# Performance work log

Hardware: AMD Instinct MI355X
Metric: run time of the kernel (lower is better)

The kernel has to match this reference:

```python
import jax, jax.numpy as jnp
import numpy as np

N_NODES = 100000
NEG_SLOPE = 0.01  # F.leaky_relu default


def _hetero_graphconv(x, src, dst, W, b, n_nodes):
    """HeteroGraphConv(aggregate='sum') of DGL GraphConv(norm='both') per edge type.

    x: [N, d_in]; src/dst: [R, E] int; W: [R, d_in, d_out]; b: [R, d_out].
    """
    n_rel = W.shape[0]
    ones = None
    out = jnp.zeros((n_nodes, W.shape[2]), dtype=x.dtype)
    for r in range(n_rel):  # small fixed number of relations
        s, d = src[r], dst[r]
        e_ones = jnp.ones(s.shape, dtype=x.dtype)
        deg_out = jnp.clip(jax.ops.segment_sum(e_ones, s, num_segments=n_nodes), 1.0)
        deg_in = jnp.clip(jax.ops.segment_sum(e_ones, d, num_segments=n_nodes), 1.0)
        # norm='both': scale src by out_deg^-1/2, aggregate, scale dst by in_deg^-1/2.
        # Apply weight before gather (aggregation is linear) to shrink edge traffic.
        h = (x * (deg_out ** -0.5)[:, None]) @ W[r]          # [N, d_out]
        agg = jax.ops.segment_sum(h[s], d, num_segments=n_nodes)  # gather-scatter over edges
        out = out + agg * (deg_in ** -0.5)[:, None] + b[r]
    return out


def setup_inputs() -> dict:
    key = jax.random.key(0)
    ks = jax.random.split(key, 8)
    d_in, d_h, d_out, n_cls, n_rel, n_edges = 256, 128, 128, 16, 3, 600000
    x = jax.random.normal(ks[0], (N_NODES, d_in), dtype=jnp.float32)
    src = jax.random.randint(ks[1], (n_rel, n_edges), 0, N_NODES, dtype=jnp.int32)
    dst = jax.random.randint(ks[2], (n_rel, n_edges), 0, N_NODES, dtype=jnp.int32)
    W0 = jax.random.normal(ks[3], (n_rel, d_in, d_h), dtype=jnp.float32) * (d_in ** -0.5)
    b0 = jnp.zeros((n_rel, d_h), dtype=jnp.float32)
    W1 = jax.random.normal(ks[4], (n_rel, d_h, d_out), dtype=jnp.float32) * (d_h ** -0.5)
    b1 = jnp.zeros((n_rel, d_out), dtype=jnp.float32)
    fc_W = jax.random.normal(ks[5], (d_out, n_cls), dtype=jnp.float32) * (d_out ** -0.5)
    fc_b = jnp.zeros((n_cls,), dtype=jnp.float32)
    return {"x": x, "src": src, "dst": dst, "W0": W0, "b0": b0,
            "W1": W1, "b1": b1, "fc_W": fc_W, "fc_b": fc_b}


def reference(x, src, dst, W0, b0, W1, b1, fc_W, fc_b):
    n = x.shape[0]
    h = _hetero_graphconv(x, src, dst, W0, b0, n)
    h = jax.nn.leaky_relu(h, negative_slope=NEG_SLOPE)  # dropout rate 0 (eval)
    h = _hetero_graphconv(h, src, dst, W1, b1, n)       # last layer: no activation
    logits = h @ fc_W + fc_b
    return (h, logits)
```

## Files before the change

### kernel.cpp

```cpp
#include <hip/hip_runtime.h>
#include <hip/hip_bf16.h>
#include <stdint.h>


typedef __attribute__((ext_vector_type(8))) short bf16x8;
typedef __attribute__((ext_vector_type(4))) float f32x4;
typedef unsigned short u16;

#define SCAN_T 256
#define SCAN_E 8
#define SCAN_BLK (SCAN_T * SCAN_E)

__global__ __launch_bounds__(256)
void hist_kernel(const int* __restrict__ src, const int* __restrict__ dst,
                 int* __restrict__ cnt_out8, int* __restrict__ cnt_in8,
                 int E, int N) {
    int e = blockIdx.x * blockDim.x + threadIdx.x;
    int r = blockIdx.y;
    if (e >= E) return;
    int copy = blockIdx.x & 7;
    size_t base = ((size_t)copy * 3 + r) * N;
    atomicAdd(cnt_out8 + base + src[(size_t)r * E + e], 1);
    atomicAdd(cnt_in8  + base + dst[(size_t)r * E + e], 1);
}

__global__ __launch_bounds__(256)
void reduce_scales_kernel(const int* __restrict__ cnt_out8, const int* __restrict__ cnt_in8,
                          float* __restrict__ s_out, float* __restrict__ s_in,
                          int* __restrict__ cnt_in, int total ) {
    int i = blockIdx.x * blockDim.x + threadIdx.x;
    if (i >= total) return;
    int co = 0, ci = 0;
#pragma unroll
    for (int c = 0; c < 8; c++) {
        co += cnt_out8[(size_t)c * total + i];
        ci += cnt_in8[(size_t)c * total + i];
    }
    s_out[i] = rsqrtf(fmaxf((float)co, 1.0f));
    s_in[i]  = rsqrtf(fmaxf((float)ci, 1.0f));
    cnt_in[i] = ci;
}

__global__ __launch_bounds__(SCAN_T)
void scan1_kernel(const int* __restrict__ cnt, int* __restrict__ pre,
                  int* __restrict__ bsums, int N) {
    int r = blockIdx.y, b = blockIdx.x, t = threadIdx.x;
    int base = b * SCAN_BLK + t * SCAN_E;
    int v[SCAN_E], s = 0;
#pragma unroll
    for (int j = 0; j < SCAN_E; j++) {
        int idx = base + j;
        v[j] = (idx < N) ? cnt[(size_t)r * N + idx] : 0;
        s += v[j];
    }
    __shared__ int sd[SCAN_T];
    sd[t] = s;
    __syncthreads();
    for (int off = 1; off < SCAN_T; off <<= 1) {
        int x = (t >= off) ? sd[t - off] : 0;
        __syncthreads();
        sd[t] += x;
        __syncthreads();
    }
    if (t == SCAN_T - 1) bsums[r * gridDim.x + b] = sd[t];
    int run = sd[t] - s;
#pragma unroll
    for (int j = 0; j < SCAN_E; j++) {
        int idx = base + j;
        if (idx < N) pre[(size_t)r * (N + 1) + idx] = run;
        run += v[j];
    }
}

__global__ void scan2_kernel(int* __restrict__ bsums, int* __restrict__ row_start,
                             int nb, int N) {
    for (int r = 0; r < 3; r++) {
        int run = 0;
        for (int b = 0; b < nb; b++) {
            int t = bsums[r * nb + b];
            bsums[r * nb + b] = run;
            run += t;
        }
        row_start[(size_t)r * (N + 1) + N] = run;
    }
}

__global__ __launch_bounds__(SCAN_T)
void scan3_kernel(int* __restrict__ pre, const int* __restrict__ bsums,
                  int* __restrict__ cursor, int nb, int N) {
    int r = blockIdx.y, b = blockIdx.x, t = threadIdx.x;
    int add = bsums[r * nb + b];
    int base = b * SCAN_BLK + t * SCAN_E;
#pragma unroll
    for (int j = 0; j < SCAN_E; j++) {
        int idx = base + j;
        if (idx < N) {
            int val = pre[(size_t)r * (N + 1) + idx] + add;
            pre[(size_t)r * (N + 1) + idx] = val;
            cursor[(size_t)r * N + idx] = val;
        }
    }
}

__global__ __launch_bounds__(256)
void bucket_fill_kernel(const int* __restrict__ src, const int* __restrict__ dst,
                        int* __restrict__ cursor, int* __restrict__ esrc,
                        int E, int N) {
    int e = blockIdx.x * blockDim.x + threadIdx.x;
    int r = blockIdx.y;
    if (e >= E) return;
    int d = dst[(size_t)r * E + e];
    int pos = atomicAdd(cursor + (size_t)r * N + d, 1);
    esrc[(size_t)r * E + pos] = src[(size_t)r * E + e];
}

__global__ __launch_bounds__(256)
void prep_w_kernel(const float* __restrict__ W0, const float* __restrict__ W1,
                   u16* __restrict__ w0hi, u16* __restrict__ w0lo,
                   u16* __restrict__ w1hi, u16* __restrict__ w1lo) {
    int idx = blockIdx.x * blockDim.x + threadIdx.x;
    const int n0 = 3 * 256 * 128;
    const int n1 = 3 * 128 * 128;
    if (idx >= n0 + n1) return;
    float f;
    u16 *phi, *plo;
    int oidx;
    if (idx < n0) {
        int r = idx / 32768, rem = idx % 32768;
        int n = rem / 256, k = rem % 256;
        f = W0[(size_t)r * 32768 + (size_t)k * 128 + n];
        phi = w0hi; plo = w0lo; oidx = idx;
    } else {
        int i2 = idx - n0;
        int r = i2 / 16384, rem = i2 % 16384;
        int n = rem / 128, k = rem % 128;
        f = W1[(size_t)r * 16384 + (size_t)k * 128 + n];
        phi = w1hi; plo = w1lo; oidx = i2;
    }
    uint32_t u = __float_as_uint(f);
    phi[oidx] = (u16)(u >> 16);
    float lo = f - __uint_as_float(u & 0xFFFF0000u);
    uint32_t ul = __float_as_uint(lo);
    plo[oidx] = (u16)((ul + 0x7FFFu + ((ul >> 16) & 1u)) >> 16);
}

__global__ __launch_bounds__(256)
void gemm_split_bf16(const float* __restrict__ A, const float* __restrict__ s_out,
                     const u16* __restrict__ Whi_all, const u16* __restrict__ Wlo_all,
                     u16* __restrict__ Cout_all, int M, int K, int Nn) {
    const int r = blockIdx.y;
    const float* scale = s_out + (size_t)r * Nn;
    const u16* Whi = Whi_all + (size_t)r * K * 128;
    const u16* Wlo = Wlo_all + (size_t)r * K * 128;
    u16* Cout = Cout_all + (size_t)r * Nn * 128;

    __shared__ u16 As_hi[128][40];
    __shared__ u16 As_lo[128][40];
    __shared__ u16 Bs_hi[128][40];
    __shared__ u16 Bs_lo[128][40];

    const int tid  = threadIdx.x;
    const int m0   = blockIdx.x * 128;
    const int lane = tid & 63;
    const int wave = tid >> 6;
    const int wm   = (wave & 1) * 64;
    const int wn   = (wave >> 1) * 64;
    const int lm   = lane & 15;
    const int kq   = (lane >> 4) * 8;

    f32x4 acc[4][4];
#pragma unroll
    for (int i = 0; i < 4; i++)
#pragma unroll
        for (int j = 0; j < 4; j++) acc[i][j] = (f32x4){0.f, 0.f, 0.f, 0.f};

    const int srow = tid >> 1;
    const int skb  = (tid & 1) * 16;

    const bool valid = (m0 + srow) < M;
    const float sval = valid ? scale[m0 + srow] : 0.f;
    const float* arow = A + (size_t)(m0 + srow) * K;
    const u16* whrow = Whi + (size_t)srow * K;
    const u16* wlrow = Wlo + (size_t)srow * K;

    for (int k0 = 0; k0 < K; k0 += 32) {
        float fa[16];
        if (valid) {
            *(float4*)&fa[0]  = *(const float4*)(arow + k0 + skb);
            *(float4*)&fa[4]  = *(const float4*)(arow + k0 + skb + 4);
            *(float4*)&fa[8]  = *(const float4*)(arow + k0 + skb + 8);
            *(float4*)&fa[12] = *(const float4*)(arow + k0 + skb + 12);
        } else {
#pragma unroll
            for (int i = 0; i < 16; i++) fa[i] = 0.f;
        }
        uint32_t ah[8], al[8];
#pragma unroll
        for (int p = 0; p < 8; p++) {
            float f0 = fa[2 * p] * sval, f1 = fa[2 * p + 1] * sval;
            uint32_t u0 = __float_as_uint(f0), u1 = __float_as_uint(f1);
            ah[p] = (u0 >> 16) | (u1 & 0xFFFF0000u);
            float l0 = f0 - __uint_as_float(u0 & 0xFFFF0000u);
            float l1 = f1 - __uint_as_float(u1 & 0xFFFF0000u);
            al[p] = (__float_as_uint(l0) >> 16) | (__float_as_uint(l1) & 0xFFFF0000u);
        }
        *(uint4*)&As_hi[srow][skb]     = *(uint4*)&ah[0];
        *(uint4*)&As_hi[srow][skb + 8] = *(uint4*)&ah[4];
        *(uint4*)&As_lo[srow][skb]     = *(uint4*)&al[0];
        *(uint4*)&As_lo[srow][skb + 8] = *(uint4*)&al[4];

        *(uint4*)&Bs_hi[srow][skb]     = *(const uint4*)(whrow + k0 + skb);
        *(uint4*)&Bs_hi[srow][skb + 8] = *(const uint4*)(whrow + k0 + skb + 8);
        *(uint4*)&Bs_lo[srow][skb]     = *(const uint4*)(wlrow + k0 + skb);
        *(uint4*)&Bs_lo[srow][skb + 8] = *(const uint4*)(wlrow + k0 + skb + 8);

        __syncthreads();

        bf16x8 a_hi[4], a_lo[4], b_hi[4], b_lo[4];
#pragma unroll
        for (int i = 0; i < 4; i++) {
            a_hi[i] = *(const bf16x8*)&As_hi[wm + i * 16 + lm][kq];
            a_lo[i] = *(const bf16x8*)&As_lo[wm + i * 16 + lm][kq];
            b_hi[i] = *(const bf16x8*)&Bs_hi[wn + i * 16 + lm][kq];
            b_lo[i] = *(const bf16x8*)&Bs_lo[wn + i * 16 + lm][kq];
        }
#pragma unroll
        for (int i = 0; i < 4; i++)
#pragma unroll
            for (int j = 0; j < 4; j++) {
                acc[i][j] = __builtin_amdgcn_mfma_f32_16x16x32_bf16(a_hi[i], b_hi[j], acc[i][j], 0, 0, 0);
                acc[i][j] = __builtin_amdgcn_mfma_f32_16x16x32_bf16(a_lo[i], b_hi[j], acc[i][j], 0, 0, 0);
                acc[i][j] = __builtin_amdgcn_mfma_f32_16x16x32_bf16(a_hi[i], b_lo[j], acc[i][j], 0, 0, 0);
            }
        __syncthreads();
    }

    const int rq = (lane >> 4) * 4;
#pragma unroll
    for (int i = 0; i < 4; i++) {
        int mbase = m0 + wm + i * 16 + rq;
#pragma unroll
        for (int j = 0; j < 4; j++) {
            int col = wn + j * 16 + lm;
#pragma unroll
            for (int rg = 0; rg < 4; rg++) {
                int m = mbase + rg;
                if (m < M) {
                    uint32_t u = __float_as_uint(acc[i][j][rg]);
                    Cout[(size_t)m * 128 + col] =
                        (u16)((u + 0x7FFFu + ((u >> 16) & 1u)) >> 16);
                }
            }
        }
    }
}

#define BF16_LO(u) __uint_as_float((u) << 16)
#define BF16_HI(u) __uint_as_float((u) & 0xFFFF0000u)

__device__ __forceinline__ void gather_rel(const uint32_t* __restrict__ h,
                                           const int* __restrict__ es,
                                           int beg, int end,
                                           float& ox, float& oy, float w) {
    float ax = 0.f, ay = 0.f, cx = 0.f, cy = 0.f;
    int e = beg;
    for (; e + 4 <= end; e += 4) {
        int s0 = es[e], s1 = es[e + 1], s2 = es[e + 2], s3 = es[e + 3];
        uint32_t u0 = h[(size_t)s0 * 64];
        uint32_t u1 = h[(size_t)s1 * 64];
        uint32_t u2 = h[(size_t)s2 * 64];
        uint32_t u3 = h[(size_t)s3 * 64];
        ax += BF16_LO(u0); ay += BF16_HI(u0);
        cx += BF16_LO(u1); cy += BF16_HI(u1);
        ax += BF16_LO(u2); ay += BF16_HI(u2);
        cx += BF16_LO(u3); cy += BF16_HI(u3);
    }
    if (e + 2 <= end) {
        int s0 = es[e], s1 = es[e + 1];
        uint32_t u0 = h[(size_t)s0 * 64];
        uint32_t u1 = h[(size_t)s1 * 64];
        ax += BF16_LO(u0); ay += BF16_HI(u0);
        cx += BF16_LO(u1); cy += BF16_HI(u1);
        e += 2;
    }
    if (e < end) {
        uint32_t u0 = h[(size_t)es[e] * 64];
        ax += BF16_LO(u0); ay += BF16_HI(u0);
    }
    ox += (ax + cx) * w;
    oy += (ay + cy) * w;
}

__global__ __launch_bounds__(256)
void gather_l0(const u16* __restrict__ hb, const int* __restrict__ row_start,
               const int* __restrict__ esrc, const float* __restrict__ s_in,
               const float* __restrict__ b, float* __restrict__ out, int N, int E) {
    int node = blockIdx.x * 4 + (threadIdx.x >> 6);
    if (node >= N) return;
    int lane = threadIdx.x & 63;
    float tx = 0.f, ty = 0.f;
#pragma unroll
    for (int r = 0; r < 3; r++) {
        const int* rs = row_start + (size_t)r * (N + 1);
        gather_rel((const uint32_t*)hb + (size_t)r * N * 64 + lane,
                   esrc + (size_t)r * E, rs[node], rs[node + 1],
                   tx, ty, s_in[(size_t)r * N + node]);
    }
    int c0 = lane * 2;
    tx += b[c0] + b[128 + c0] + b[256 + c0];
    ty += b[c0 + 1] + b[128 + c0 + 1] + b[256 + c0 + 1];
    tx = fmaxf(tx, 0.f) + 0.01f * fminf(tx, 0.f);
    ty = fmaxf(ty, 0.f) + 0.01f * fminf(ty, 0.f);
    *(float2*)(out + (size_t)node * 128 + c0) = make_float2(tx, ty);
}

__global__ __launch_bounds__(256)
void gather_l1(const u16* __restrict__ hb, const int* __restrict__ row_start,
               const int* __restrict__ esrc, const float* __restrict__ s_in,
               const float* __restrict__ b, const float* __restrict__ fcW,
               const float* __restrict__ fcb, float* __restrict__ out_h,
               float* __restrict__ out_logits, int N, int E) {
    int node = blockIdx.x * 4 + (threadIdx.x >> 6);
    if (node >= N) return;
    int lane = threadIdx.x & 63;
    float tx = 0.f, ty = 0.f;
#pragma unroll
    for (int r = 0; r < 3; r++) {
        const int* rs = row_start + (size_t)r * (N + 1);
        gather_rel((const uint32_t*)hb + (size_t)r * N * 64 + lane,
                   esrc + (size_t)r * E, rs[node], rs[node + 1],
                   tx, ty, s_in[(size_t)r * N + node]);
    }
    int c0 = lane * 2;
    tx += b[c0] + b[128 + c0] + b[256 + c0];
    ty += b[c0 + 1] + b[128 + c0 + 1] + b[256 + c0 + 1];
    *(float2*)(out_h + (size_t)node * 128 + c0) = make_float2(tx, ty);

    const float* fc0 = fcW + (size_t)c0 * 16;
    float p[16];
#pragma unroll
    for (int j = 0; j < 16; j++) p[j] = tx * fc0[j] + ty * fc0[16 + j];
#pragma unroll
    for (int off = 1; off < 64; off <<= 1) {
#pragma unroll
        for (int j = 0; j < 16; j++) p[j] += __shfl_xor(p[j], off);
    }
    if (lane == 0) {
        float* lp = out_logits + (size_t)node * 16;
        *(float4*)(lp + 0)  = make_float4(p[0] + fcb[0],  p[1] + fcb[1],  p[2] + fcb[2],  p[3] + fcb[3]);
        *(float4*)(lp + 4)  = make_float4(p[4] + fcb[4],  p[5] + fcb[5],  p[6] + fcb[6],  p[7] + fcb[7]);
        *(float4*)(lp + 8)  = make_float4(p[8] + fcb[8],  p[9] + fcb[9],  p[10] + fcb[10], p[11] + fcb[11]);
        *(float4*)(lp + 12) = make_float4(p[12] + fcb[12], p[13] + fcb[13], p[14] + fcb[14], p[15] + fcb[15]);
    }
}

extern "C" void kernel_launch(void* const* d_in, const int* in_sizes, int n_in,
                              void* d_out, int out_size, void* d_ws, size_t ws_size,
                              hipStream_t stream) {
    const float* x   = (const float*)d_in[0];
    const int*   src = (const int*)d_in[1];
    const int*   dst = (const int*)d_in[2];
    const float* W0  = (const float*)d_in[3];
    const float* b0  = (const float*)d_in[4];
    const float* W1  = (const float*)d_in[5];
    const float* b1  = (const float*)d_in[6];
    const float* fcW = (const float*)d_in[7];
    const float* fcb = (const float*)d_in[8];

    const int N = in_sizes[0] / 256;
    const int E = in_sizes[1] / 3;
    const int nb = (N + SCAN_BLK - 1) / SCAN_BLK;

    float* out_h      = (float*)d_out;
    float* out_logits = out_h + (size_t)N * 128;

    char* p = (char*)d_ws;
    auto alloc = [&](size_t bytes) -> char* {
        char* q = p;
        p += (bytes + 255) & ~(size_t)255;
        return q;
    };
    float* s_out     = (float*)alloc(3 * (size_t)N * 4);
    float* s_in      = (float*)alloc(3 * (size_t)N * 4);
    int*   cnt8      = (int*)alloc(2 * 8 * 3 * (size_t)N * 4);
    int*   cnt_out8  = cnt8;
    int*   cnt_in8   = cnt8 + 8 * 3 * (size_t)N;
    int*   cnt_in    = (int*)alloc(3 * (size_t)N * 4);
    int*   row_start = (int*)alloc(3 * (size_t)(N + 1) * 4);
    int*   cursor    = (int*)alloc(3 * (size_t)N * 4);
    int*   bsums     = (int*)alloc(1024 * 4);
    int*   esrc      = (int*)alloc(3 * (size_t)E * 4);
    u16*   w0hi      = (u16*)alloc(3 * 256 * 128 * 2);
    u16*   w0lo      = (u16*)alloc(3 * 256 * 128 * 2);
    u16*   w1hi      = (u16*)alloc(3 * 128 * 128 * 2);
    u16*   w1lo      = (u16*)alloc(3 * 128 * 128 * 2);
    u16*   hb        = (u16*)alloc(3 * (size_t)N * 128 * 2);
    float* acc0      = (float*)alloc((size_t)N * 128 * 4);

    hipMemsetAsync(cnt8, 0, 2 * 8 * 3 * (size_t)N * sizeof(int), stream);

    hist_kernel<<<dim3((E + 255) / 256, 3), 256, 0, stream>>>(src, dst, cnt_out8, cnt_in8, E, N);
    reduce_scales_kernel<<<(3 * N + 255) / 256, 256, 0, stream>>>(
        cnt_out8, cnt_in8, s_out, s_in, cnt_in, 3 * N);

    scan1_kernel<<<dim3(nb, 3), SCAN_T, 0, stream>>>(cnt_in, row_start, bsums, N);
    scan2_kernel<<<1, 1, 0, stream>>>(bsums, row_start, nb, N);
    scan3_kernel<<<dim3(nb, 3), SCAN_T, 0, stream>>>(row_start, bsums, cursor, nb, N);
    bucket_fill_kernel<<<dim3((E + 255) / 256, 3), 256, 0, stream>>>(src, dst, cursor, esrc, E, N);

    prep_w_kernel<<<(3 * 256 * 128 + 3 * 128 * 128 + 255) / 256, 256, 0, stream>>>(
        W0, W1, w0hi, w0lo, w1hi, w1lo);

    int gemm_blocks   = (N + 127) / 128;
    int gather_blocks = (N + 3) / 4;

    gemm_split_bf16<<<dim3(gemm_blocks, 3), 256, 0, stream>>>(
        x, s_out, w0hi, w0lo, hb, N, 256, N);
    gather_l0<<<gather_blocks, 256, 0, stream>>>(hb, row_start, esrc, s_in, b0, acc0, N, E);

    gemm_split_bf16<<<dim3(gemm_blocks, 3), 256, 0, stream>>>(
        acc0, s_out, w1hi, w1lo, hb, N, 128, N);
    gather_l1<<<gather_blocks, 256, 0, stream>>>(hb, row_start, esrc, s_in, b1, fcW, fcb,
                                                 out_h, out_logits, N, E);
}
```

Measured before the change: 842.6 us.

## Merge per-relation CSR into one combined CSR and gather two edges per wave

Builds a single CSR over all three relations keyed by destination, storing a global row index (r*N+src) per edge, so the scan and cursor arrays shrink to one relation. The gather loads edge indices cooperatively with one coalesced load per 64 edges, broadcasts them via shuffles, and has each half-wave fetch 8-byte chunks of different source rows, then combines halves with a shuffle. Per-relation in-degree scaling is chosen per edge from the index range. This aims to raise memory-level parallelism and cut index-load overhead in the gather, at the cost of extra shuffles and select logic, and a different summation order.

```diff
diff --git a/kernel.cpp b/kernel.cpp
--- a/kernel.cpp
+++ b/kernel.cpp
@@ -27,30 +27,35 @@
 __global__ __launch_bounds__(256)
 void reduce_scales_kernel(const int* __restrict__ cnt_out8, const int* __restrict__ cnt_in8,
                           float* __restrict__ s_out, float* __restrict__ s_in,
-                          int* __restrict__ cnt_in, int total ) {
-    int i = blockIdx.x * blockDim.x + threadIdx.x;
-    if (i >= total) return;
-    int co = 0, ci = 0;
-#pragma unroll
-    for (int c = 0; c < 8; c++) {
-        co += cnt_out8[(size_t)c * total + i];
-        ci += cnt_in8[(size_t)c * total + i];
-    }
-    s_out[i] = rsqrtf(fmaxf((float)co, 1.0f));
-    s_in[i]  = rsqrtf(fmaxf((float)ci, 1.0f));
-    cnt_in[i] = ci;
+                          int* __restrict__ cnt_all, int N) {
+    int n = blockIdx.x * blockDim.x + threadIdx.x;
+    if (n >= N) return;
+    int tot = 0;
+#pragma unroll
+    for (int r = 0; r < 3; r++) {
+        int co = 0, ci = 0;
+#pragma unroll
+        for (int c = 0; c < 8; c++) {
+            co += cnt_out8[((size_t)c * 3 + r) * N + n];
+            ci += cnt_in8[((size_t)c * 3 + r) * N + n];
+        }
+        s_out[(size_t)r * N + n] = rsqrtf(fmaxf((float)co, 1.0f));
+        s_in[(size_t)r * N + n]  = rsqrtf(fmaxf((float)ci, 1.0f));
+        tot += ci;
+    }
+    cnt_all[n] = tot;
 }
 
 __global__ __launch_bounds__(SCAN_T)
 void scan1_kernel(const int* __restrict__ cnt, int* __restrict__ pre,
                   int* __restrict__ bsums, int N) {
-    int r = blockIdx.y, b = blockIdx.x, t = threadIdx.x;
+    int b = blockIdx.x, t = threadIdx.x;
     int base = b * SCAN_BLK + t * SCAN_E;
     int v[SCAN_E], s = 0;
 #pragma unroll
     for (int j = 0; j < SCAN_E; j++) {
         int idx = base + j;
-        v[j] = (idx < N) ? cnt[(size_t)r * N + idx] : 0;
+        v[j] = (idx < N) ? cnt[idx] : 0;
         s += v[j];
     }
     __shared__ int sd[SCAN_T];
@@ -62,42 +67,40 @@
         sd[t] += x;
         __syncthreads();
     }
-    if (t == SCAN_T - 1) bsums[r * gridDim.x + b] = sd[t];
+    if (t == SCAN_T - 1) bsums[b] = sd[t];
     int run = sd[t] - s;
 #pragma unroll
     for (int j = 0; j < SCAN_E; j++) {
         int idx = base + j;
-        if (idx < N) pre[(size_t)r * (N + 1) + idx] = run;
+        if (idx < N) pre[idx] = run;
         run += v[j];
     }
 }
 
 __global__ void scan2_kernel(int* __restrict__ bsums, int* __restrict__ row_start,
                              int nb, int N) {
-    for (int r = 0; r < 3; r++) {
-        int run = 0;
-        for (int b = 0; b < nb; b++) {
-            int t = bsums[r * nb + b];
-            bsums[r * nb + b] = run;
-            run += t;
-        }
-        row_start[(size_t)r * (N + 1) + N] = run;
-    }
+    int run = 0;
+    for (int b = 0; b < nb; b++) {
+        int t = bsums[b];
+        bsums[b] = run;
+        run += t;
+    }
+    row_start[N] = run;
 }
 
 __global__ __launch_bounds__(SCAN_T)
 void scan3_kernel(int* __restrict__ pre, const int* __restrict__ bsums,
                   int* __restrict__ cursor, int nb, int N) {
-    int r = blockIdx.y, b = blockIdx.x, t = threadIdx.x;
-    int add = bsums[r * nb + b];
+    int b = blockIdx.x, t = threadIdx.x;
+    int add = bsums[b];
     int base = b * SCAN_BLK + t * SCAN_E;
 #pragma unroll
     for (int j = 0; j < SCAN_E; j++) {
         int idx = base + j;
         if (idx < N) {
-            int val = pre[(size_t)r * (N + 1) + idx] + add;
-            pre[(size_t)r * (N + 1) + idx] = val;
-            cursor[(size_t)r * N + idx] = val;
+            int val = pre[idx] + add;
+            pre[idx] = val;
+            cursor[idx] = val;
         }
     }
 }
@@ -110,8 +113,8 @@
     int r = blockIdx.y;
     if (e >= E) return;
     int d = dst[(size_t)r * E + e];
-    int pos = atomicAdd(cursor + (size_t)r * N + d, 1);
-    esrc[(size_t)r * E + pos] = src[(size_t)r * E + e];
+    int pos = atomicAdd(cursor + d, 1);
+    esrc[pos] = r * N + src[(size_t)r * E + e];
 }
 
 __global__ __launch_bounds__(256)
@@ -255,63 +258,69 @@
     }
 }
 
-#define BF16_LO(u) __uint_as_float((u) << 16)
-#define BF16_HI(u) __uint_as_float((u) & 0xFFFF0000u)
-
-__device__ __forceinline__ void gather_rel(const uint32_t* __restrict__ h,
-                                           const int* __restrict__ es,
-                                           int beg, int end,
-                                           float& ox, float& oy, float w) {
-    float ax = 0.f, ay = 0.f, cx = 0.f, cy = 0.f;
-    int e = beg;
-    for (; e + 4 <= end; e += 4) {
-        int s0 = es[e], s1 = es[e + 1], s2 = es[e + 2], s3 = es[e + 3];
-        uint32_t u0 = h[(size_t)s0 * 64];
-        uint32_t u1 = h[(size_t)s1 * 64];
-        uint32_t u2 = h[(size_t)s2 * 64];
-        uint32_t u3 = h[(size_t)s3 * 64];
-        ax += BF16_LO(u0); ay += BF16_HI(u0);
-        cx += BF16_LO(u1); cy += BF16_HI(u1);
-        ax += BF16_LO(u2); ay += BF16_HI(u2);
-        cx += BF16_LO(u3); cy += BF16_HI(u3);
-    }
-    if (e + 2 <= end) {
-        int s0 = es[e], s1 = es[e + 1];
-        uint32_t u0 = h[(size_t)s0 * 64];
-        uint32_t u1 = h[(size_t)s1 * 64];
-        ax += BF16_LO(u0); ay += BF16_HI(u0);
-        cx += BF16_LO(u1); cy += BF16_HI(u1);
-        e += 2;
-    }
-    if (e < end) {
-        uint32_t u0 = h[(size_t)es[e] * 64];
-        ax += BF16_LO(u0); ay += BF16_HI(u0);
-    }
-    ox += (ax + cx) * w;
-    oy += (ay + cy) * w;
+__device__ __forceinline__ void gather_all(const u16* __restrict__ hb,
+                                           const int* __restrict__ row_start,
+                                           const int* __restrict__ esrc,
+                                           const float* __restrict__ s_in,
+                                           int node, int lane, int N,
+                                           float acc[4]) {
+    const uint32_t* hrow = (const uint32_t*)hb + (lane & 31) * 2;
+    const int slot = lane >> 5;
+    const int N2 = N * 2;
+    const float w0 = s_in[node];
+    const float w1 = s_in[(size_t)N + node];
+    const float w2 = s_in[(size_t)N2 + node];
+    const int beg = row_start[node];
+    const int end = row_start[node + 1];
+    acc[0] = acc[1] = acc[2] = acc[3] = 0.f;
+    for (int base = beg; base < end; base += 64) {
+        int cn = end - base;
+        cn = cn > 64 ? 64 : cn;
+        int cidx = esrc[base + lane];
+        for (int j = 0; j < cn; j += 8) {
+            uint2 u[4];
+            float w[4];
+#pragma unroll
+            for (int p = 0; p < 4; p++) {
+                int jj = j + 2 * p + slot;
+                int idx = __shfl(cidx, jj);
+                float ws = (idx >= N) ? ((idx >= N2) ? w2 : w1) : w0;
+                bool act = jj < cn;
+                w[p] = act ? ws : 0.f;
+                idx = act ? idx : 0;
+                u[p] = *(const uint2*)(hrow + (size_t)idx * 64);
+            }
+#pragma unroll
+            for (int p = 0; p < 4; p++) {
+                acc[0] = fmaf(__uint_as_float(u[p].x << 16),          w[p], acc[0]);
+                acc[1] = fmaf(__uint_as_float(u[p].x & 0xFFFF0000u),  w[p], acc[1]);
+                acc[2] = fmaf(__uint_as_float(u[p].y << 16),          w[p], acc[2]);
+                acc[3] = fmaf(__uint_as_float(u[p].y & 0xFFFF0000u),  w[p], acc[3]);
+            }
+        }
+    }
+#pragma unroll
+    for (int k = 0; k < 4; k++) acc[k] += __shfl_xor(acc[k], 32);
 }
 
 __global__ __launch_bounds__(256)
 void gather_l0(const u16* __restrict__ hb, const int* __restrict__ row_start,
                const int* __restrict__ esrc, const float* __restrict__ s_in,
-               const float* __restrict__ b, float* __restrict__ out, int N, int E) {
+               const float* __restrict__ b, float* __restrict__ out, int N) {
     int node = blockIdx.x * 4 + (threadIdx.x >> 6);
     if (node >= N) return;
     int lane = threadIdx.x & 63;
-    float tx = 0.f, ty = 0.f;
-#pragma unroll
-    for (int r = 0; r < 3; r++) {
-        const int* rs = row_start + (size_t)r * (N + 1);
-        gather_rel((const uint32_t*)hb + (size_t)r * N * 64 + lane,
-                   esrc + (size_t)r * E, rs[node], rs[node + 1],
-                   tx, ty, s_in[(size_t)r * N + node]);
-    }
-    int c0 = lane * 2;
-    tx += b[c0] + b[128 + c0] + b[256 + c0];
-    ty += b[c0 + 1] + b[128 + c0 + 1] + b[256 + c0 + 1];
-    tx = fmaxf(tx, 0.f) + 0.01f * fminf(tx, 0.f);
-    ty = fmaxf(ty, 0.f) + 0.01f * fminf(ty, 0.f);
-    *(float2*)(out + (size_t)node * 128 + c0) = make_float2(tx, ty);
+    float acc[4];
+    gather_all(hb, row_start, esrc, s_in, node, lane, N, acc);
+    int c0 = (lane & 31) * 4;
+    float4 o;
+    float* po = (float*)&o;
+#pragma unroll
+    for (int k = 0; k < 4; k++) {
+        float v = acc[k] + b[c0 + k] + b[128 + c0 + k] + b[256 + c0 + k];
+        po[k] = fmaxf(v, 0.f) + 0.01f * fminf(v, 0.f);
+    }
+    if (lane < 32) *(float4*)(out + (size_t)node * 128 + c0) = o;
 }
 
 __global__ __launch_bounds__(256)
@@ -319,31 +328,34 @@
                const int* __restrict__ esrc, const float* __restrict__ s_in,
                const float* __restrict__ b, const float* __restrict__ fcW,
                const float* __restrict__ fcb, float* __restrict__ out_h,
-               float* __restrict__ out_logits, int N, int E) {
+               float* __restrict__ out_logits, int N) {
     int node = blockIdx.x * 4 + (threadIdx.x >> 6);
     if (node >= N) return;
     int lane = threadIdx.x & 63;
-    float tx = 0.f, ty = 0.f;
-#pragma unroll
-    for (int r = 0; r < 3; r++) {
-        const int* rs = row_start + (size_t)r * (N + 1);
-        gather_rel((const uint32_t*)hb + (size_t)r * N * 64 + lane,
-                   esrc + (size_t)r * E, rs[node], rs[node + 1],
-                   tx, ty, s_in[(size_t)r * N + node]);
-    }
-    int c0 = lane * 2;
-    tx += b[c0] + b[128 + c0] + b[256 + c0];
-    ty += b[c0 + 1] + b[128 + c0 + 1] + b[256 + c0 + 1];
-    *(float2*)(out_h + (size_t)node * 128 + c0) = make_float2(tx, ty);
-
-    const float* fc0 = fcW + (size_t)c0 * 16;
+    float acc[4];
+    gather_all(hb, row_start, esrc, s_in, node, lane, N, acc);
+    int c0 = (lane & 31) * 4;
+    float v[4];
+#pragma unroll
+    for (int k = 0; k < 4; k++)
+        v[k] = acc[k] + b[c0 + k] + b[128 + c0 + k] + b[256 + c0 + k];
+    if (lane < 32) {
+        float4 o = make_float4(v[0], v[1], v[2], v[3]);
+        *(float4*)(out_h + (size_t)node * 128 + c0) = o;
+    }
+
     float p[16];
 #pragma unroll
-    for (int j = 0; j < 16; j++) p[j] = tx * fc0[j] + ty * fc0[16 + j];
-#pragma unroll
-    for (int off = 1; off < 64; off <<= 1) {
-#pragma unroll
-        for (int j = 0; j < 16; j++) p[j] += __shfl_xor(p[j], off);
+    for (int jj = 0; jj < 16; jj++) {
+        p[jj] = v[0] * fcW[(size_t)(c0 + 0) * 16 + jj]
+              + v[1] * fcW[(size_t)(c0 + 1) * 16 + jj]
+              + v[2] * fcW[(size_t)(c0 + 2) * 16 + jj]
+              + v[3] * fcW[(size_t)(c0 + 3) * 16 + jj];
+    }
+#pragma unroll
+    for (int off = 1; off <= 16; off <<= 1) {
+#pragma unroll
+        for (int jj = 0; jj < 16; jj++) p[jj] += __shfl_xor(p[jj], off);
     }
     if (lane == 0) {
         float* lp = out_logits + (size_t)node * 16;
@@ -385,11 +397,11 @@
     int*   cnt8      = (int*)alloc(2 * 8 * 3 * (size_t)N * 4);
     int*   cnt_out8  = cnt8;
     int*   cnt_in8   = cnt8 + 8 * 3 * (size_t)N;
-    int*   cnt_in    = (int*)alloc(3 * (size_t)N * 4);
-    int*   row_start = (int*)alloc(3 * (size_t)(N + 1) * 4);
-    int*   cursor    = (int*)alloc(3 * (size_t)N * 4);
+    int*   cnt_all   = (int*)alloc((size_t)N * 4);
+    int*   row_start = (int*)alloc((size_t)(N + 1) * 4);
+    int*   cursor    = (int*)alloc((size_t)N * 4);
     int*   bsums     = (int*)alloc(1024 * 4);
-    int*   esrc      = (int*)alloc(3 * (size_t)E * 4);
+    int*   esrc      = (int*)alloc(3 * (size_t)E * 4 + 256);
     u16*   w0hi      = (u16*)alloc(3 * 256 * 128 * 2);
     u16*   w0lo      = (u16*)alloc(3 * 256 * 128 * 2);
     u16*   w1hi      = (u16*)alloc(3 * 128 * 128 * 2);
@@ -400,12 +412,12 @@
     hipMemsetAsync(cnt8, 0, 2 * 8 * 3 * (size_t)N * sizeof(int), stream);
 
     hist_kernel<<<dim3((E + 255) / 256, 3), 256, 0, stream>>>(src, dst, cnt_out8, cnt_in8, E, N);
-    reduce_scales_kernel<<<(3 * N + 255) / 256, 256, 0, stream>>>(
-        cnt_out8, cnt_in8, s_out, s_in, cnt_in, 3 * N);
-
-    scan1_kernel<<<dim3(nb, 3), SCAN_T, 0, stream>>>(cnt_in, row_start, bsums, N);
+    reduce_scales_kernel<<<(N + 255) / 256, 256, 0, stream>>>(
+        cnt_out8, cnt_in8, s_out, s_in, cnt_all, N);
+
+    scan1_kernel<<<nb, SCAN_T, 0, stream>>>(cnt_all, row_start, bsums, N);
     scan2_kernel<<<1, 1, 0, stream>>>(bsums, row_start, nb, N);
-    scan3_kernel<<<dim3(nb, 3), SCAN_T, 0, stream>>>(row_start, bsums, cursor, nb, N);
+    scan3_kernel<<<nb, SCAN_T, 0, stream>>>(row_start, bsums, cursor, nb, N);
     bucket_fill_kernel<<<dim3((E + 255) / 256, 3), 256, 0, stream>>>(src, dst, cursor, esrc, E, N);
 
     prep_w_kernel<<<(3 * 256 * 128 + 3 * 128 * 128 + 255) / 256, 256, 0, stream>>>(
@@ -416,10 +428,10 @@
 
     gemm_split_bf16<<<dim3(gemm_blocks, 3), 256, 0, stream>>>(
         x, s_out, w0hi, w0lo, hb, N, 256, N);
-    gather_l0<<<gather_blocks, 256, 0, stream>>>(hb, row_start, esrc, s_in, b0, acc0, N, E);
+    gather_l0<<<gather_blocks, 256, 0, stream>>>(hb, row_start, esrc, s_in, b0, acc0, N);
 
     gemm_split_bf16<<<dim3(gemm_blocks, 3), 256, 0, stream>>>(
         acc0, s_out, w1hi, w1lo, hb, N, 128, N);
     gather_l1<<<gather_blocks, 256, 0, stream>>>(hb, row_start, esrc, s_in, b1, fcW, fcb,
-                                                 out_h, out_logits, N, E);
-}
+                                                 out_h, out_logits, N);
+}
```

After: 899.7 us. +6.8%, slower.
